# Performance work log

Measured on AMD Instinct MI355X. Metric: run time of the kernel, lower is better.

## Reference

```python
import jax, jax.numpy as jnp
import numpy as np
from jax import lax

TAGSET_SIZE = 64
START_TAG = TAGSET_SIZE - 2
STOP_TAG = TAGSET_SIZE - 1
NEG_INF = -10000.0


def setup_inputs() -> dict:
    key = jax.random.key(0)
    k_feat, k_trans, k_tags = jax.random.split(key, 3)
    B, S, T = 512, 1024, TAGSET_SIZE
    feats = jax.random.normal(k_feat, (B, S, T), dtype=jnp.float32)
    transitions = jax.random.normal(k_trans, (T, T), dtype=jnp.float32)
    # CRF constraints: nothing transitions FROM anything into START row semantics
    # of the torch code: transitions[START, :] = -1e4 ; transitions[:, STOP] = -1e4
    transitions = transitions.at[START_TAG, :].set(NEG_INF)
    transitions = transitions.at[:, STOP_TAG].set(NEG_INF)
    tags = jax.random.randint(k_tags, (B, S), 0, T - 2, dtype=jnp.int64)
    mask = jnp.ones((B, S), dtype=jnp.int32)
    return {"feats": feats, "transitions": transitions, "tags": tags, "mask": mask}


def _forward_alg(feats, transitions, maskf):
    # feats: (B,S,T), maskf: (B,S) float
    B, S, T = feats.shape
    init = jnp.full((B, T), NEG_INF, dtype=feats.dtype).at[:, START_TAG].set(0.0)

    def step(fv, xs):
        feat, m = xs  # feat: (B,T), m: (B,)
        # next_tag_var[b, next, prev] = fv[b,prev] + trans[next,prev] + feat[b,next]
        nxt = jax.nn.logsumexp(
            fv[:, None, :] + transitions[None, :, :] + feat[:, :, None], axis=2
        )
        m1 = m[:, None]
        return nxt * m1 + fv * (1.0 - m1), None

    fv, _ = lax.scan(step, init, (feats.transpose(1, 0, 2), maskf.T))
    terminal = fv + transitions[STOP_TAG][None, :]
    return jax.nn.logsumexp(terminal, axis=1)  # (B,)


def _score_sentence(feats, transitions, tags, maskf):
    B, S, T = feats.shape
    tags_ext = jnp.concatenate(
        [jnp.full((B, 1), START_TAG, dtype=tags.dtype), tags], axis=1
    )  # (B, S+1)
    cur = tags_ext[:, 1:]   # (B,S)
    prev = tags_ext[:, :-1]  # (B,S)
    emit = jnp.take_along_axis(feats, cur[:, :, None], axis=2)[:, :, 0]  # (B,S)
    trans = transitions[cur, prev]  # (B,S)
    score = jnp.sum((emit + trans) * maskf, axis=1)
    last_idx = maskf.sum(axis=1).astype(jnp.int32)  # index into tags_ext
    last_tags = jnp.take_along_axis(tags_ext, last_idx[:, None].astype(tags.dtype), axis=1)[:, 0]
    return score + transitions[STOP_TAG, last_tags]


def reference(feats, transitions, tags, mask):
    maskf = mask.astype(feats.dtype)
    forward_score = _forward_alg(feats, transitions, maskf)
    gold_score = _score_sentence(feats, transitions, tags, maskf)
    return jnp.mean(forward_score - gold_score)
```

## Files before the change

kernel.cpp:

```cpp
#include <hip/hip_runtime.h>

#define TAGS 64
#define START_TAG 62
#define STOP_TAG 63
#define BATCH 512
#define SLEN 1024
#define HALF 512
#define NGROUP 32

typedef float vf4 __attribute__((ext_vector_type(4)));
typedef short short8 __attribute__((ext_vector_type(8)));

__device__ __forceinline__ unsigned pk_bf16(float lo, float hi) {
  return __builtin_amdgcn_perm(__float_as_uint(hi), __float_as_uint(lo), 0x07060302u);
}
__device__ __forceinline__ short bf16_rne(float x) {
  unsigned u = __float_as_uint(x);
  u += 0x7FFFu + ((u >> 16) & 1u);
  return (short)(u >> 16);
}

__global__ __launch_bounds__(128, 1)
void crf_main(const float* __restrict__ feats, const float* __restrict__ trans,
              const int* __restrict__ tags, const int* __restrict__ mask,
              float* __restrict__ ws) {
  __shared__ float shl[64 * 17 + 32];
  const int blk = blockIdx.x;
  const int lane = threadIdx.x & 63;
  const int wave = threadIdx.x >> 6;

  if (blk < NGROUP) {
    const int g = blk;
    const int q = lane >> 4;
    const int col = lane & 15;
    const int b = g * 16 + col;
    const float* fb = feats + (size_t)b * (SLEN * TAGS) + q * 16;
    const int* mb = mask + b * SLEN;

    short8 A[4][2];
    const int mrow = 16 * (col >> 2) + (col & 3);
    #pragma unroll
    for (int t = 0; t < 4; ++t) {
      #pragma unroll
      for (int c = 0; c < 2; ++c) {
        short8 a;
        #pragma unroll
        for (int j = 0; j < 8; ++j) {
          int R = mrow + 4 * t;
          int K = 16 * q + 8 * c + j;
          float tv = (wave == 0) ? trans[R * 64 + K] : trans[K * 64 + R];
          a[j] = bf16_rne(__expf(tv));
        }
        A[t][c] = a;
      }
    }

    float W[16];
    float C = 0.f;

    if (wave == 0) {
      #pragma unroll
      for (int i = 0; i < 16; ++i) W[i] = 0.f;
      if (q == 3) W[14] = 1.f;

      vf4 pf[4][4];
      #pragma unroll
      for (int u = 0; u < 4; ++u)
        #pragma unroll
        for (int v = 0; v < 4; ++v) pf[u][v] = *(const vf4*)(fb + u * 64 + v * 4);
      int4 mc = *(const int4*)(mb);

      for (int k = 0; k < HALF / 4; ++k) {
        int4 mn = (k < HALF / 4 - 1) ? *(const int4*)(mb + 4 * k + 8 - 4) : make_int4(1, 1, 1, 1);
        int allm = mc.x & mc.y & mc.z & mc.w;
        bool fastp = (__ballot(allm != 0) == ~0ull);
        #pragma unroll
        for (int u = 0; u < 4; ++u) {
          union { unsigned uu[4]; short8 s; } B0, B1;
          B0.uu[0] = pk_bf16(W[0], W[1]);   B0.uu[1] = pk_bf16(W[2], W[3]);
          B0.uu[2] = pk_bf16(W[4], W[5]);   B0.uu[3] = pk_bf16(W[6], W[7]);
          B1.uu[0] = pk_bf16(W[8], W[9]);   B1.uu[1] = pk_bf16(W[10], W[11]);
          B1.uu[2] = pk_bf16(W[12], W[13]); B1.uu[3] = pk_bf16(W[14], W[15]);
          vf4 z4 = {0.f, 0.f, 0.f, 0.f};
          vf4 d0 = __builtin_amdgcn_mfma_f32_16x16x32_bf16(A[0][0], B0.s, z4, 0, 0, 0);
          vf4 d1 = __builtin_amdgcn_mfma_f32_16x16x32_bf16(A[1][0], B0.s, z4, 0, 0, 0);
          vf4 d2 = __builtin_amdgcn_mfma_f32_16x16x32_bf16(A[2][0], B0.s, z4, 0, 0, 0);
          vf4 d3 = __builtin_amdgcn_mfma_f32_16x16x32_bf16(A[3][0], B0.s, z4, 0, 0, 0);
          d0 = __builtin_amdgcn_mfma_f32_16x16x32_bf16(A[0][1], B1.s, d0, 0, 0, 0);
          d1 = __builtin_amdgcn_mfma_f32_16x16x32_bf16(A[1][1], B1.s, d1, 0, 0, 0);
          d2 = __builtin_amdgcn_mfma_f32_16x16x32_bf16(A[2][1], B1.s, d2, 0, 0, 0);
          d3 = __builtin_amdgcn_mfma_f32_16x16x32_bf16(A[3][1], B1.s, d3, 0, 0, 0);
          vf4 f0 = pf[u][0], f1 = pf[u][1], f2 = pf[u][2], f3 = pf[u][3];
          int s = 4 * k + u;
          #pragma unroll
          for (int v = 0; v < 4; ++v) pf[u][v] = *(const vf4*)(fb + (s + 4) * 64 + v * 4);
          if (fastp) {
            #pragma unroll
            for (int i = 0; i < 4; ++i) {
              W[i]      = d0[i] * __expf(f0[i]);
              W[4 + i]  = d1[i] * __expf(f1[i]);
              W[8 + i]  = d2[i] * __expf(f2[i]);
              W[12 + i] = d3[i] * __expf(f3[i]);
            }
          } else {
            int mv = (u == 0) ? mc.x : (u == 1) ? mc.y : (u == 2) ? mc.z : mc.w;
            #pragma unroll
            for (int i = 0; i < 4; ++i) {
              W[i]      = mv ? d0[i] * __expf(f0[i]) : W[i];
              W[4 + i]  = mv ? d1[i] * __expf(f1[i]) : W[4 + i];
              W[8 + i]  = mv ? d2[i] * __expf(f2[i]) : W[8 + i];
              W[12 + i] = mv ? d3[i] * __expf(f3[i]) : W[12 + i];
            }
          }
        }
        float z = __shfl(W[0], col);
        float rz = __builtin_amdgcn_rcpf(z);
        C += __logf(z);
        #pragma unroll
        for (int i = 0; i < 16; ++i) W[i] *= rz;
        mc = mn;
      }
    } else {
      #pragma unroll
      for (int i = 0; i < 16; ++i) W[i] = __expf(trans[STOP_TAG * 64 + (16 * q + i)]);

      vf4 pf[4][4];
      #pragma unroll
      for (int u = 0; u < 4; ++u)
        #pragma unroll
        for (int v = 0; v < 4; ++v) pf[u][v] = *(const vf4*)(fb + (1023 - u) * 64 + v * 4);
      int4 mc = *(const int4*)(mb + 1020);

      for (int k = 0; k < HALF / 4; ++k) {
        int4 mn = (k < HALF / 4 - 1) ? *(const int4*)(mb + 1020 - 4 * (k + 1)) : make_int4(1, 1, 1, 1);
        int allm = mc.x & mc.y & mc.z & mc.w;
        bool fastp = (__ballot(allm != 0) == ~0ull);
        #pragma unroll
        for (int u = 0; u < 4; ++u) {
          vf4 f0 = pf[u][0], f1 = pf[u][1], f2 = pf[u][2], f3 = pf[u][3];
          int s = 1023 - 4 * k - u;
          #pragma unroll
          for (int v = 0; v < 4; ++v) pf[u][v] = *(const vf4*)(fb + (s - 4) * 64 + v * 4);
          float Wt[16];
          #pragma unroll
          for (int i = 0; i < 4; ++i) {
            Wt[i]      = W[i]      * __expf(f0[i]);
            Wt[4 + i]  = W[4 + i]  * __expf(f1[i]);
            Wt[8 + i]  = W[8 + i]  * __expf(f2[i]);
            Wt[12 + i] = W[12 + i] * __expf(f3[i]);
          }
          union { unsigned uu[4]; short8 s8; } B0, B1;
          B0.uu[0] = pk_bf16(Wt[0], Wt[1]);   B0.uu[1] = pk_bf16(Wt[2], Wt[3]);
          B0.uu[2] = pk_bf16(Wt[4], Wt[5]);   B0.uu[3] = pk_bf16(Wt[6], Wt[7]);
          B1.uu[0] = pk_bf16(Wt[8], Wt[9]);   B1.uu[1] = pk_bf16(Wt[10], Wt[11]);
          B1.uu[2] = pk_bf16(Wt[12], Wt[13]); B1.uu[3] = pk_bf16(Wt[14], Wt[15]);
          vf4 z4 = {0.f, 0.f, 0.f, 0.f};
          vf4 d0 = __builtin_amdgcn_mfma_f32_16x16x32_bf16(A[0][0], B0.s8, z4, 0, 0, 0);
          vf4 d1 = __builtin_amdgcn_mfma_f32_16x16x32_bf16(A[1][0], B0.s8, z4, 0, 0, 0);
          vf4 d2 = __builtin_amdgcn_mfma_f32_16x16x32_bf16(A[2][0], B0.s8, z4, 0, 0, 0);
          vf4 d3 = __builtin_amdgcn_mfma_f32_16x16x32_bf16(A[3][0], B0.s8, z4, 0, 0, 0);
          d0 = __builtin_amdgcn_mfma_f32_16x16x32_bf16(A[0][1], B1.s8, d0, 0, 0, 0);
          d1 = __builtin_amdgcn_mfma_f32_16x16x32_bf16(A[1][1], B1.s8, d1, 0, 0, 0);
          d2 = __builtin_amdgcn_mfma_f32_16x16x32_bf16(A[2][1], B1.s8, d2, 0, 0, 0);
          d3 = __builtin_amdgcn_mfma_f32_16x16x32_bf16(A[3][1], B1.s8, d3, 0, 0, 0);
          if (fastp) {
            #pragma unroll
            for (int i = 0; i < 4; ++i) {
              W[i] = d0[i]; W[4 + i] = d1[i]; W[8 + i] = d2[i]; W[12 + i] = d3[i];
            }
          } else {
            int mv = (u == 0) ? mc.w : (u == 1) ? mc.z : (u == 2) ? mc.y : mc.x;
            #pragma unroll
            for (int i = 0; i < 4; ++i) {
              W[i]      = mv ? d0[i] : W[i];
              W[4 + i]  = mv ? d1[i] : W[4 + i];
              W[8 + i]  = mv ? d2[i] : W[8 + i];
              W[12 + i] = mv ? d3[i] : W[12 + i];
            }
          }
        }
        float z = __shfl(W[0], col);
        float rz = __builtin_amdgcn_rcpf(z);
        C += __logf(z);
        #pragma unroll
        for (int i = 0; i < 16; ++i) W[i] *= rz;
        mc = mn;
      }
    }

    if (wave == 1) {
      #pragma unroll
      for (int i = 0; i < 16; ++i) shl[lane * 17 + i] = W[i];
      shl[lane * 17 + 16] = C;
    }
    __syncthreads();
    if (wave == 0) {
      float p = 0.f;
      #pragma unroll
      for (int i = 0; i < 16; ++i) p += W[i] * shl[lane * 17 + i];
      p += __shfl_xor(p, 16);
      p += __shfl_xor(p, 32);
      float sc = C + shl[lane * 17 + 16] + __logf(p);
      if (lane < 16) ws[b] = sc;
    }
    (void)tags;
  } else {
    const int b = blk - NGROUP;
    const int* tb = tags + b * SLEN;
    const int* mb = mask + b * SLEN;
    const float* fbg = feats + (size_t)b * SLEN * TAGS;
    float acc = 0.f, cnt = 0.f;
    const int t = threadIdx.x;
    for (int k = 0; k < SLEN / 128; ++k) {
      int s = t + k * 128;
      int cur = tb[s];
      int prev = (s == 0) ? START_TAG : tb[s - 1];
      float m = (float)mb[s];
      acc += m * (fbg[s * 64 + cur] + trans[cur * 64 + prev]);
      cnt += m;
    }
    shl[t] = acc;
    shl[128 + t] = cnt;
    __syncthreads();
    if (t == 0) {
      float a = 0.f, c = 0.f;
      for (int i = 0; i < 128; ++i) { a += shl[i]; c += shl[128 + i]; }
      int last_idx = (int)(c + 0.5f);
      int last_tag = (last_idx == 0) ? START_TAG : tb[last_idx - 1];
      ws[BATCH + b] = a + trans[STOP_TAG * 64 + last_tag];
    }
  }
}

__global__ __launch_bounds__(512)
void crf_reduce(const float* __restrict__ ws, float* __restrict__ out) {
  __shared__ float s[512];
  const int t = threadIdx.x;
  s[t] = ws[t] - ws[BATCH + t];
  __syncthreads();
  for (int off = 256; off > 0; off >>= 1) {
    if (t < off) s[t] += s[t + off];
    __syncthreads();
  }
  if (t == 0) out[0] = s[0] * (1.f / (float)BATCH);
}

extern "C" void kernel_launch(void* const* d_in, const int* in_sizes, int n_in,
                              void* d_out, int out_size, void* d_ws, size_t ws_size,
                              hipStream_t stream) {
  const float* feats = (const float*)d_in[0];
  const float* trans = (const float*)d_in[1];
  const int* tags = (const int*)d_in[2];
  const int* mask = (const int*)d_in[3];
  float* ws = (float*)d_ws;
  float* out = (float*)d_out;

  crf_main<<<NGROUP + BATCH, 128, 0, stream>>>(feats, trans, tags, mask, ws);
  crf_reduce<<<1, 512, 0, stream>>>(ws, out);
}
```

Measured before the change: 374.1 us.

## Split CRF chains into per-direction blocks with async LDS ring prefetch

The forward and backward half-chains now run in separate single-wave blocks, so each gets its own CU, instead of sharing one two-wave block. The all-ones mask path streams feats through a 12-slot LDS ring filled with global_load_lds, and a precheck of the mask picks either this path or the masked path. Combining the two halves moves into the reduce kernel through workspace. The gold-score blocks switch to 64 threads with a shuffle reduction. This is meant to hide per-step global load latency on the serial recurrence, at the cost of a heavier reduce kernel and hand-tuned vmcnt waits that must match the number of loads in flight.

```diff
diff --git a/kernel.cpp b/kernel.cpp
--- a/kernel.cpp
+++ b/kernel.cpp
@@ -1,12 +1,15 @@
 #include <hip/hip_runtime.h>
 
-#define TAGS 64
 #define START_TAG 62
 #define STOP_TAG 63
 #define BATCH 512
 #define SLEN 1024
-#define HALF 512
-#define NGROUP 32
+#define NG 32
+#define NCHAIN 64
+#define RD 12
+#define AH 8
+#define SLOTB 4096
+#define RINGB (RD * SLOTB)
 
 typedef float vf4 __attribute__((ext_vector_type(4)));
 typedef short short8 __attribute__((ext_vector_type(8)));
@@ -19,215 +22,211 @@
   u += 0x7FFFu + ((u >> 16) & 1u);
   return (short)(u >> 16);
 }
-
-__global__ __launch_bounds__(128, 1)
+__device__ __forceinline__ vf4 mfma16(short8 a, short8 b, vf4 c) {
+  return __builtin_amdgcn_mfma_f32_16x16x32_bf16(a, b, c, 0, 0, 0);
+}
+__device__ __forceinline__ void async16(const void* g, void* l) {
+  __builtin_amdgcn_global_load_lds((const __attribute__((address_space(1))) unsigned*)g,
+                                   (__attribute__((address_space(3))) unsigned*)l, 16, 0, 0);
+}
+
+template<int DIR, bool MASKED>
+__device__ __forceinline__ void chain_run(const float* __restrict__ feats,
+                                          const float* __restrict__ trans,
+                                          const int* __restrict__ mask,
+                                          float* __restrict__ ws, char* smem, int g) {
+  const int lane = threadIdx.x & 63;
+  const int q = lane >> 4, col = lane & 15;
+  const int b = g * 16 + col;
+
+  short8 A[4][2];
+  const int mrow = 16 * (col >> 2) + (col & 3);
+  #pragma unroll
+  for (int t = 0; t < 4; ++t) {
+    #pragma unroll
+    for (int c = 0; c < 2; ++c) {
+      short8 a;
+      #pragma unroll
+      for (int j = 0; j < 8; ++j) {
+        int R = mrow + 4 * t, K = 16 * q + 8 * c + j;
+        float tv = (DIR == 0) ? trans[R * 64 + K] : trans[K * 64 + R];
+        a[j] = bf16_rne(__expf(tv));
+      }
+      A[t][c] = a;
+    }
+  }
+
+  float W[16];
+  float C = 0.f;
+  if (DIR == 0) {
+    #pragma unroll
+    for (int i = 0; i < 16; ++i) W[i] = 0.f;
+    if (q == 3) W[14] = 1.f;
+  } else {
+    #pragma unroll
+    for (int i = 0; i < 16; ++i) W[i] = __expf(trans[STOP_TAG * 64 + 16 * q + i]);
+  }
+
+  const char* gb = (const char*)feats + (size_t)b * 262144 + (size_t)q * 64;
+
+  vf4 cur[4];
+  int rOff = 0, wOff = 0;
+  if constexpr (!MASKED) {
+    asm volatile("s_waitcnt vmcnt(0)" ::: "memory");
+    #pragma unroll
+    for (int p = 0; p < AH; ++p) {
+      int s = (DIR == 0) ? p : 1023 - p;
+      #pragma unroll
+      for (int v = 0; v < 4; ++v)
+        async16(gb + (size_t)s * 256 + v * 16, smem + p * SLOTB + v * 1024);
+    }
+    wOff = AH * SLOTB;
+    asm volatile("s_waitcnt vmcnt(28)" ::: "memory");
+    #pragma unroll
+    for (int v = 0; v < 4; ++v)
+      cur[v] = *(const vf4*)(smem + v * 1024 + lane * 16);
+    rOff = SLOTB;
+  } else {
+    int s0 = (DIR == 0) ? 0 : 1023;
+    #pragma unroll
+    for (int v = 0; v < 4; ++v)
+      cur[v] = *(const vf4*)(gb + (size_t)s0 * 256 + v * 16);
+  }
+
+  for (int grp = 0; grp < 128; ++grp) {
+    #pragma unroll
+    for (int u = 0; u < 4; ++u) {
+      const int j = grp * 4 + u;
+      float e[16];
+      #pragma unroll
+      for (int v = 0; v < 4; ++v)
+        #pragma unroll
+        for (int i = 0; i < 4; ++i) e[v * 4 + i] = __expf(cur[v][i]);
+
+      float P[16];
+      #pragma unroll
+      for (int i = 0; i < 16; ++i) P[i] = (DIR == 0) ? W[i] : W[i] * e[i];
+
+      union { unsigned uu[4]; short8 s8; } B0, B1;
+      B0.uu[0] = pk_bf16(P[0], P[1]);   B0.uu[1] = pk_bf16(P[2], P[3]);
+      B0.uu[2] = pk_bf16(P[4], P[5]);   B0.uu[3] = pk_bf16(P[6], P[7]);
+      B1.uu[0] = pk_bf16(P[8], P[9]);   B1.uu[1] = pk_bf16(P[10], P[11]);
+      B1.uu[2] = pk_bf16(P[12], P[13]); B1.uu[3] = pk_bf16(P[14], P[15]);
+
+      vf4 z4 = {0.f, 0.f, 0.f, 0.f};
+      vf4 d0 = mfma16(A[0][0], B0.s8, z4);
+      vf4 d1 = mfma16(A[1][0], B0.s8, z4);
+      vf4 d2 = mfma16(A[2][0], B0.s8, z4);
+      vf4 d3 = mfma16(A[3][0], B0.s8, z4);
+      d0 = mfma16(A[0][1], B1.s8, d0);
+      d1 = mfma16(A[1][1], B1.s8, d1);
+      d2 = mfma16(A[2][1], B1.s8, d2);
+      d3 = mfma16(A[3][1], B1.s8, d3);
+
+      int m = 1;
+      if constexpr (!MASKED) {
+        asm volatile("s_waitcnt vmcnt(24)" ::: "memory");
+        #pragma unroll
+        for (int v = 0; v < 4; ++v)
+          cur[v] = *(const vf4*)(smem + rOff + v * 1024 + lane * 16);
+        rOff += SLOTB; if (rOff == RINGB) rOff = 0;
+        int jp = j + AH; if (jp > 511) jp = 511;
+        int sp = (DIR == 0) ? jp : 1023 - jp;
+        #pragma unroll
+        for (int v = 0; v < 4; ++v)
+          async16(gb + (size_t)sp * 256 + v * 16, smem + wOff + v * 1024);
+        wOff += SLOTB; if (wOff == RINGB) wOff = 0;
+      } else {
+        int sj = (DIR == 0) ? j : 1023 - j;
+        m = mask[b * 1024 + sj];
+        int sn = (DIR == 0) ? (j + 1) : 1023 - (j + 1);
+        #pragma unroll
+        for (int v = 0; v < 4; ++v)
+          cur[v] = *(const vf4*)(gb + (size_t)sn * 256 + v * 16);
+      }
+
+      #pragma unroll
+      for (int i = 0; i < 4; ++i) {
+        float n0 = (DIR == 0) ? d0[i] * e[i]      : d0[i];
+        float n1 = (DIR == 0) ? d1[i] * e[4 + i]  : d1[i];
+        float n2 = (DIR == 0) ? d2[i] * e[8 + i]  : d2[i];
+        float n3 = (DIR == 0) ? d3[i] * e[12 + i] : d3[i];
+        if (MASKED) {
+          W[i]      = m ? n0 : W[i];
+          W[4 + i]  = m ? n1 : W[4 + i];
+          W[8 + i]  = m ? n2 : W[8 + i];
+          W[12 + i] = m ? n3 : W[12 + i];
+        } else {
+          W[i] = n0; W[4 + i] = n1; W[8 + i] = n2; W[12 + i] = n3;
+        }
+      }
+    }
+    float z = __shfl(W[0], col);
+    float rz = __builtin_amdgcn_rcpf(z);
+    C += __logf(z);
+    #pragma unroll
+    for (int i = 0; i < 16; ++i) W[i] *= rz;
+  }
+
+  float* slab = ws + (size_t)(g * 2 + DIR) * 1024;
+  #pragma unroll
+  for (int t4 = 0; t4 < 4; ++t4) {
+    vf4 o = {W[t4 * 4], W[t4 * 4 + 1], W[t4 * 4 + 2], W[t4 * 4 + 3]};
+    *(vf4*)(slab + lane * 16 + t4 * 4) = o;
+  }
+  if (q == 0) ws[65536 + (g * 2 + DIR) * 16 + col] = C;
+}
+
+__global__ __launch_bounds__(64, 1)
 void crf_main(const float* __restrict__ feats, const float* __restrict__ trans,
               const int* __restrict__ tags, const int* __restrict__ mask,
               float* __restrict__ ws) {
-  __shared__ float shl[64 * 17 + 32];
+  __shared__ char smem[RINGB];
   const int blk = blockIdx.x;
-  const int lane = threadIdx.x & 63;
-  const int wave = threadIdx.x >> 6;
-
-  if (blk < NGROUP) {
-    const int g = blk;
-    const int q = lane >> 4;
-    const int col = lane & 15;
+  if (blk < NCHAIN) {
+    const int g = blk >> 1, dir = blk & 1;
+    const int lane = threadIdx.x & 63;
+    const int q = lane >> 4, col = lane & 15;
     const int b = g * 16 + col;
-    const float* fb = feats + (size_t)b * (SLEN * TAGS) + q * 16;
-    const int* mb = mask + b * SLEN;
-
-    short8 A[4][2];
-    const int mrow = 16 * (col >> 2) + (col & 3);
-    #pragma unroll
-    for (int t = 0; t < 4; ++t) {
-      #pragma unroll
-      for (int c = 0; c < 2; ++c) {
-        short8 a;
-        #pragma unroll
-        for (int j = 0; j < 8; ++j) {
-          int R = mrow + 4 * t;
-          int K = 16 * q + 8 * c + j;
-          float tv = (wave == 0) ? trans[R * 64 + K] : trans[K * 64 + R];
-          a[j] = bf16_rne(__expf(tv));
-        }
-        A[t][c] = a;
-      }
-    }
-
-    float W[16];
-    float C = 0.f;
-
-    if (wave == 0) {
-      #pragma unroll
-      for (int i = 0; i < 16; ++i) W[i] = 0.f;
-      if (q == 3) W[14] = 1.f;
-
-      vf4 pf[4][4];
-      #pragma unroll
-      for (int u = 0; u < 4; ++u)
-        #pragma unroll
-        for (int v = 0; v < 4; ++v) pf[u][v] = *(const vf4*)(fb + u * 64 + v * 4);
-      int4 mc = *(const int4*)(mb);
-
-      for (int k = 0; k < HALF / 4; ++k) {
-        int4 mn = (k < HALF / 4 - 1) ? *(const int4*)(mb + 4 * k + 8 - 4) : make_int4(1, 1, 1, 1);
-        int allm = mc.x & mc.y & mc.z & mc.w;
-        bool fastp = (__ballot(allm != 0) == ~0ull);
-        #pragma unroll
-        for (int u = 0; u < 4; ++u) {
-          union { unsigned uu[4]; short8 s; } B0, B1;
-          B0.uu[0] = pk_bf16(W[0], W[1]);   B0.uu[1] = pk_bf16(W[2], W[3]);
-          B0.uu[2] = pk_bf16(W[4], W[5]);   B0.uu[3] = pk_bf16(W[6], W[7]);
-          B1.uu[0] = pk_bf16(W[8], W[9]);   B1.uu[1] = pk_bf16(W[10], W[11]);
-          B1.uu[2] = pk_bf16(W[12], W[13]); B1.uu[3] = pk_bf16(W[14], W[15]);
-          vf4 z4 = {0.f, 0.f, 0.f, 0.f};
-          vf4 d0 = __builtin_amdgcn_mfma_f32_16x16x32_bf16(A[0][0], B0.s, z4, 0, 0, 0);
-          vf4 d1 = __builtin_amdgcn_mfma_f32_16x16x32_bf16(A[1][0], B0.s, z4, 0, 0, 0);
-          vf4 d2 = __builtin_amdgcn_mfma_f32_16x16x32_bf16(A[2][0], B0.s, z4, 0, 0, 0);
-          vf4 d3 = __builtin_amdgcn_mfma_f32_16x16x32_bf16(A[3][0], B0.s, z4, 0, 0, 0);
-          d0 = __builtin_amdgcn_mfma_f32_16x16x32_bf16(A[0][1], B1.s, d0, 0, 0, 0);
-          d1 = __builtin_amdgcn_mfma_f32_16x16x32_bf16(A[1][1], B1.s, d1, 0, 0, 0);
-          d2 = __builtin_amdgcn_mfma_f32_16x16x32_bf16(A[2][1], B1.s, d2, 0, 0, 0);
-          d3 = __builtin_amdgcn_mfma_f32_16x16x32_bf16(A[3][1], B1.s, d3, 0, 0, 0);
-          vf4 f0 = pf[u][0], f1 = pf[u][1], f2 = pf[u][2], f3 = pf[u][3];
-          int s = 4 * k + u;
-          #pragma unroll
-          for (int v = 0; v < 4; ++v) pf[u][v] = *(const vf4*)(fb + (s + 4) * 64 + v * 4);
-          if (fastp) {
-            #pragma unroll
-            for (int i = 0; i < 4; ++i) {
-              W[i]      = d0[i] * __expf(f0[i]);
-              W[4 + i]  = d1[i] * __expf(f1[i]);
-              W[8 + i]  = d2[i] * __expf(f2[i]);
-              W[12 + i] = d3[i] * __expf(f3[i]);
-            }
-          } else {
-            int mv = (u == 0) ? mc.x : (u == 1) ? mc.y : (u == 2) ? mc.z : mc.w;
-            #pragma unroll
-            for (int i = 0; i < 4; ++i) {
-              W[i]      = mv ? d0[i] * __expf(f0[i]) : W[i];
-              W[4 + i]  = mv ? d1[i] * __expf(f1[i]) : W[4 + i];
-              W[8 + i]  = mv ? d2[i] * __expf(f2[i]) : W[8 + i];
-              W[12 + i] = mv ? d3[i] * __expf(f3[i]) : W[12 + i];
-            }
-          }
-        }
-        float z = __shfl(W[0], col);
-        float rz = __builtin_amdgcn_rcpf(z);
-        C += __logf(z);
-        #pragma unroll
-        for (int i = 0; i < 16; ++i) W[i] *= rz;
-        mc = mn;
-      }
+    const int sB = dir ? 512 : 0;
+    int anyz = 0;
+    for (int it = 0; it < 32; ++it) {
+      int4 v = *(const int4*)(mask + b * 1024 + sB + (it * 4 + q) * 4);
+      anyz |= (v.x == 0) | (v.y == 0) | (v.z == 0) | (v.w == 0);
+    }
+    bool allones = (__ballot(anyz != 0) == 0ull);
+    if (allones) {
+      if (dir == 0) chain_run<0, false>(feats, trans, mask, ws, smem, g);
+      else          chain_run<1, false>(feats, trans, mask, ws, smem, g);
     } else {
-      #pragma unroll
-      for (int i = 0; i < 16; ++i) W[i] = __expf(trans[STOP_TAG * 64 + (16 * q + i)]);
-
-      vf4 pf[4][4];
-      #pragma unroll
-      for (int u = 0; u < 4; ++u)
-        #pragma unroll
-        for (int v = 0; v < 4; ++v) pf[u][v] = *(const vf4*)(fb + (1023 - u) * 64 + v * 4);
-      int4 mc = *(const int4*)(mb + 1020);
-
-      for (int k = 0; k < HALF / 4; ++k) {
-        int4 mn = (k < HALF / 4 - 1) ? *(const int4*)(mb + 1020 - 4 * (k + 1)) : make_int4(1, 1, 1, 1);
-        int allm = mc.x & mc.y & mc.z & mc.w;
-        bool fastp = (__ballot(allm != 0) == ~0ull);
-        #pragma unroll
-        for (int u = 0; u < 4; ++u) {
-          vf4 f0 = pf[u][0], f1 = pf[u][1], f2 = pf[u][2], f3 = pf[u][3];
-          int s = 1023 - 4 * k - u;
-          #pragma unroll
-          for (int v = 0; v < 4; ++v) pf[u][v] = *(const vf4*)(fb + (s - 4) * 64 + v * 4);
-          float Wt[16];
-          #pragma unroll
-          for (int i = 0; i < 4; ++i) {
-            Wt[i]      = W[i]      * __expf(f0[i]);
-            Wt[4 + i]  = W[4 + i]  * __expf(f1[i]);
-            Wt[8 + i]  = W[8 + i]  * __expf(f2[i]);
-            Wt[12 + i] = W[12 + i] * __expf(f3[i]);
-          }
-          union { unsigned uu[4]; short8 s8; } B0, B1;
-          B0.uu[0] = pk_bf16(Wt[0], Wt[1]);   B0.uu[1] = pk_bf16(Wt[2], Wt[3]);
-          B0.uu[2] = pk_bf16(Wt[4], Wt[5]);   B0.uu[3] = pk_bf16(Wt[6], Wt[7]);
-          B1.uu[0] = pk_bf16(Wt[8], Wt[9]);   B1.uu[1] = pk_bf16(Wt[10], Wt[11]);
-          B1.uu[2] = pk_bf16(Wt[12], Wt[13]); B1.uu[3] = pk_bf16(Wt[14], Wt[15]);
-          vf4 z4 = {0.f, 0.f, 0.f, 0.f};
-          vf4 d0 = __builtin_amdgcn_mfma_f32_16x16x32_bf16(A[0][0], B0.s8, z4, 0, 0, 0);
-          vf4 d1 = __builtin_amdgcn_mfma_f32_16x16x32_bf16(A[1][0], B0.s8, z4, 0, 0, 0);
-          vf4 d2 = __builtin_amdgcn_mfma_f32_16x16x32_bf16(A[2][0], B0.s8, z4, 0, 0, 0);
-          vf4 d3 = __builtin_amdgcn_mfma_f32_16x16x32_bf16(A[3][0], B0.s8, z4, 0, 0, 0);
-          d0 = __builtin_amdgcn_mfma_f32_16x16x32_bf16(A[0][1], B1.s8, d0, 0, 0, 0);
-          d1 = __builtin_amdgcn_mfma_f32_16x16x32_bf16(A[1][1], B1.s8, d1, 0, 0, 0);
-          d2 = __builtin_amdgcn_mfma_f32_16x16x32_bf16(A[2][1], B1.s8, d2, 0, 0, 0);
-          d3 = __builtin_amdgcn_mfma_f32_16x16x32_bf16(A[3][1], B1.s8, d3, 0, 0, 0);
-          if (fastp) {
-            #pragma unroll
-            for (int i = 0; i < 4; ++i) {
-              W[i] = d0[i]; W[4 + i] = d1[i]; W[8 + i] = d2[i]; W[12 + i] = d3[i];
-            }
-          } else {
-            int mv = (u == 0) ? mc.w : (u == 1) ? mc.z : (u == 2) ? mc.y : mc.x;
-            #pragma unroll
-            for (int i = 0; i < 4; ++i) {
-              W[i]      = mv ? d0[i] : W[i];
-              W[4 + i]  = mv ? d1[i] : W[4 + i];
-              W[8 + i]  = mv ? d2[i] : W[8 + i];
-              W[12 + i] = mv ? d3[i] : W[12 + i];
-            }
-          }
-        }
-        float z = __shfl(W[0], col);
-        float rz = __builtin_amdgcn_rcpf(z);
-        C += __logf(z);
-        #pragma unroll
-        for (int i = 0; i < 16; ++i) W[i] *= rz;
-        mc = mn;
-      }
-    }
-
-    if (wave == 1) {
-      #pragma unroll
-      for (int i = 0; i < 16; ++i) shl[lane * 17 + i] = W[i];
-      shl[lane * 17 + 16] = C;
-    }
-    __syncthreads();
-    if (wave == 0) {
-      float p = 0.f;
-      #pragma unroll
-      for (int i = 0; i < 16; ++i) p += W[i] * shl[lane * 17 + i];
-      p += __shfl_xor(p, 16);
-      p += __shfl_xor(p, 32);
-      float sc = C + shl[lane * 17 + 16] + __logf(p);
-      if (lane < 16) ws[b] = sc;
+      if (dir == 0) chain_run<0, true>(feats, trans, mask, ws, smem, g);
+      else          chain_run<1, true>(feats, trans, mask, ws, smem, g);
     }
     (void)tags;
   } else {
-    const int b = blk - NGROUP;
+    const int b = blk - NCHAIN;
     const int* tb = tags + b * SLEN;
     const int* mb = mask + b * SLEN;
-    const float* fbg = feats + (size_t)b * SLEN * TAGS;
+    const float* fbg = feats + (size_t)b * 65536;
     float acc = 0.f, cnt = 0.f;
     const int t = threadIdx.x;
-    for (int k = 0; k < SLEN / 128; ++k) {
-      int s = t + k * 128;
+    for (int k = 0; k < 16; ++k) {
+      int s = t + k * 64;
       int cur = tb[s];
       int prev = (s == 0) ? START_TAG : tb[s - 1];
       float m = (float)mb[s];
       acc += m * (fbg[s * 64 + cur] + trans[cur * 64 + prev]);
       cnt += m;
     }
-    shl[t] = acc;
-    shl[128 + t] = cnt;
-    __syncthreads();
+    #pragma unroll
+    for (int o = 1; o < 64; o <<= 1) {
+      acc += __shfl_xor(acc, o);
+      cnt += __shfl_xor(cnt, o);
+    }
     if (t == 0) {
-      float a = 0.f, c = 0.f;
-      for (int i = 0; i < 128; ++i) { a += shl[i]; c += shl[128 + i]; }
-      int last_idx = (int)(c + 0.5f);
+      int last_idx = (int)(cnt + 0.5f);
       int last_tag = (last_idx == 0) ? START_TAG : tb[last_idx - 1];
-      ws[BATCH + b] = a + trans[STOP_TAG * 64 + last_tag];
+      ws[66560 + b] = acc + trans[STOP_TAG * 64 + last_tag];
     }
   }
 }
@@ -236,13 +235,23 @@
 void crf_reduce(const float* __restrict__ ws, float* __restrict__ out) {
   __shared__ float s[512];
   const int t = threadIdx.x;
-  s[t] = ws[t] - ws[BATCH + t];
+  const int g = t >> 4, col = t & 15;
+  const float* Wf = ws + (size_t)(2 * g) * 1024;
+  const float* Wb = ws + (size_t)(2 * g + 1) * 1024;
+  float P = 0.f;
+  #pragma unroll
+  for (int q = 0; q < 4; ++q)
+    #pragma unroll
+    for (int i = 0; i < 16; ++i)
+      P += Wf[(q * 16 + col) * 16 + i] * Wb[(q * 16 + col) * 16 + i];
+  float sc = ws[65536 + (2 * g) * 16 + col] + ws[65536 + (2 * g + 1) * 16 + col] + __logf(P);
+  s[t] = sc - ws[66560 + t];
   __syncthreads();
   for (int off = 256; off > 0; off >>= 1) {
     if (t < off) s[t] += s[t + off];
     __syncthreads();
   }
-  if (t == 0) out[0] = s[0] * (1.f / (float)BATCH);
+  if (t == 0) out[0] = s[0] * (1.f / 512.f);
 }
 
 extern "C" void kernel_launch(void* const* d_in, const int* in_sizes, int n_in,
@@ -255,6 +264,6 @@
   float* ws = (float*)d_ws;
   float* out = (float*)d_out;
 
-  crf_main<<<NGROUP + BATCH, 128, 0, stream>>>(feats, trans, tags, mask, ws);
+  crf_main<<<NCHAIN + BATCH, 64, 0, stream>>>(feats, trans, tags, mask, ws);
   crf_reduce<<<1, 512, 0, stream>>>(ws, out);
 }
```

Measured after the change: 309.6 us. -17.3%, faster.
